# Kernel optimization log

Measured on AMD Instinct MI355X. Metric: run time of the kernel, lower is better.

## Reference

```python
import jax, jax.numpy as jnp
import numpy as np

B, N, D = 1024, 100000, 512


def setup_inputs() -> dict:
    key = jax.random.key(0)
    k1, k2, k3 = jax.random.split(key, 3)
    x_t = jax.random.normal(k1, (B, D), dtype=jnp.float32)
    # keep t away from 0/1 so b_t = 1 - t is well conditioned
    t = jax.random.uniform(k2, (B,), dtype=jnp.float32, minval=0.05, maxval=0.95)
    dataset = jax.random.normal(k3, (N, D), dtype=jnp.float32)
    return {"x_t": x_t, "t": t, "dataset": dataset}


def reference(x_t, t, dataset):
    # Straight-line AffineInterp: a_t = t, b_t = 1 - t, dot_a = 1, dot_b = -1.
    # Original detaches coeffs (detach=True).
    a_t = jax.lax.stop_gradient(t)
    b_t = jax.lax.stop_gradient(1.0 - t)
    dot_a_t = jnp.ones_like(a_t)
    dot_b_t = -jnp.ones_like(b_t)

    dataset_norm = jnp.sum(dataset * dataset, axis=1)          # (N,)
    term_1 = jnp.sum(x_t * x_t, axis=1)                        # (B,)
    term_2 = jnp.einsum('bd,nd->bn', x_t, dataset)             # (B, N)

    # ||x_t - a_t * x1||^2 expanded, scaled by -1/(2 b_t^2)
    logit = (term_1[:, None]
             - 2.0 * a_t[:, None] * term_2
             + (a_t * a_t)[:, None] * dataset_norm[None, :])
    logit = (-1.0 / (2.0 * b_t * b_t))[:, None] * logit        # (B, N)

    prob = jax.nn.softmax(logit, axis=1)                       # (B, N)
    data_coeff = dot_a_t - a_t * dot_b_t / b_t                 # (B,)
    prob = prob * data_coeff[:, None]

    weighted_dataset = jnp.einsum('bn,nd->bd', prob, dataset)  # (B, D)
    v = (dot_b_t / b_t)[:, None] * x_t + weighted_dataset
    return v
```

## Files before the change

### kernel.cpp

```cpp
#include <hip/hip_runtime.h>
#include <math.h>

#define B_SZ 1024
#define N_SZ 100000
#define D_SZ 512
#define NBLK 3125

typedef __attribute__((ext_vector_type(8))) short short8;
typedef __attribute__((ext_vector_type(16))) float float16;

__device__ __forceinline__ unsigned f2bf(float x) {
    unsigned u = __float_as_uint(x);
    u += 0x7FFFu + ((u >> 16) & 1u);
    return u >> 16;
}
__device__ __forceinline__ float bf2f(unsigned h) {
    return __uint_as_float(h << 16);
}

__global__ __launch_bounds__(256) void pre_kernel(
    const float* __restrict__ ds, const float* __restrict__ x_t,
    short* __restrict__ Yh, short* __restrict__ Yl, short* __restrict__ Yt,
    short* __restrict__ Xh, short* __restrict__ Xl, float* __restrict__ norms)
{
    __shared__ unsigned short YS[32 * 512];
    const int bx = blockIdx.x, tid = threadIdx.x;
    if (bx < NBLK) {
        const int row = tid >> 3, seg = tid & 7;
        const size_t g = (size_t)(bx * 32 + row) * 512 + seg * 64;
        const int ls = row * 512 + seg * 64;
        float nrm = 0.f;
        #pragma unroll
        for (int i = 0; i < 16; i++) {
            float4 v = *(const float4*)(ds + g + i * 4);
            nrm += v.x*v.x + v.y*v.y + v.z*v.z + v.w*v.w;
            unsigned h0 = f2bf(v.x), h1 = f2bf(v.y), h2 = f2bf(v.z), h3 = f2bf(v.w);
            unsigned l0 = f2bf(v.x - bf2f(h0)), l1 = f2bf(v.y - bf2f(h1));
            unsigned l2 = f2bf(v.z - bf2f(h2)), l3 = f2bf(v.w - bf2f(h3));
            uint2 hw = make_uint2(h0 | (h1 << 16), h2 | (h3 << 16));
            uint2 lw = make_uint2(l0 | (l1 << 16), l2 | (l3 << 16));
            *(uint2*)(Yh + g + i * 4) = hw;
            *(uint2*)(Yl + g + i * 4) = lw;
            *(uint2*)(YS + ls + i * 4) = hw;
        }
        nrm += __shfl_xor(nrm, 1, 64);
        nrm += __shfl_xor(nrm, 2, 64);
        nrm += __shfl_xor(nrm, 4, 64);
        if ((tid & 7) == 0) norms[bx * 32 + row] = nrm;
        __syncthreads();
        #pragma unroll
        for (int r = 0; r < 2; r++) {
            const int d = tid + r * 256;
            unsigned w[16];
            #pragma unroll
            for (int j = 0; j < 16; j++) {
                unsigned lo = YS[(2 * j) * 512 + d];
                unsigned hi = YS[(2 * j + 1) * 512 + d];
                w[j] = lo | (hi << 16);
            }
            uint4* dst = (uint4*)(Yt + (size_t)bx * 16384 + d * 32);
            dst[0] = make_uint4(w[0], w[1], w[2], w[3]);
            dst[1] = make_uint4(w[4], w[5], w[6], w[7]);
            dst[2] = make_uint4(w[8], w[9], w[10], w[11]);
            dst[3] = make_uint4(w[12], w[13], w[14], w[15]);
        }
    } else {
        const int xb = bx - NBLK;
        #pragma unroll
        for (int k = 0; k < 16; k++) {
            const size_t i4 = (size_t)xb * 4096 + k * 256 + tid;
            float4 v = *(const float4*)(x_t + i4 * 4);
            unsigned h0 = f2bf(v.x), h1 = f2bf(v.y), h2 = f2bf(v.z), h3 = f2bf(v.w);
            unsigned l0 = f2bf(v.x - bf2f(h0)), l1 = f2bf(v.y - bf2f(h1));
            unsigned l2 = f2bf(v.z - bf2f(h2)), l3 = f2bf(v.w - bf2f(h3));
            *(uint2*)(Xh + i4 * 4) = make_uint2(h0 | (h1 << 16), h2 | (h3 << 16));
            *(uint2*)(Xl + i4 * 4) = make_uint2(l0 | (l1 << 16), l2 | (l3 << 16));
        }
    }
}

__global__ __launch_bounds__(512, 2) void attn_kernel(
    const float* __restrict__ t,
    const short* __restrict__ Xh, const short* __restrict__ Xl,
    const short* __restrict__ Yh, const short* __restrict__ Yl,
    const short* __restrict__ Yt, const float* __restrict__ norms,
    float* __restrict__ m_part, float* __restrict__ l_part,
    float* __restrict__ acc_part, int chunk)
{
    __shared__ short YhL[32 * 512];
    __shared__ short YlL[32 * 512];
    __shared__ float slots[4 * 64 * 33];
    __shared__ float Pbuf[64 * 36];
    __shared__ float c1A[64], c2A[64], mAs[64], lAs[64], alA[64];
    __shared__ float nrmL[32];

    const int tid = threadIdx.x;
    const int wave = tid >> 6, lane = tid & 63;
    const int half = lane >> 5, l31 = lane & 31;

    int qbi = blockIdx.x, si = blockIdx.y;
    if (gridDim.x == 16 && gridDim.y == 16) {
        int fid = blockIdx.x + (blockIdx.y << 4);
        int xcd = fid & 7, slot = fid >> 3;
        si = xcd + ((slot & 1) << 3);
        qbi = slot >> 1;
    }
    const int qb = qbi * 64;
    const int s = si;
    const int n0s = s * chunk;
    const int n1 = min(N_SZ, n0s + chunk);
    const int numTiles = (n1 - n0s + 31) >> 5;

    if (tid < 64) {
        float tv = t[qb + tid];
        float bt = 1.0f - tv;
        float i2 = 1.0f / (2.0f * bt * bt);
        c1A[tid] = 2.0f * tv * i2;
        c2A[tid] = tv * tv * i2;
        mAs[tid] = -1e30f;
        lAs[tid] = 0.0f;
        alA[tid] = 0.0f;
    }
    __syncthreads();

    if (wave < 4) {
        short8 XF[2][8][2];
        #pragma unroll
        for (int qt = 0; qt < 2; qt++)
            #pragma unroll
            for (int kc = 0; kc < 8; kc++) {
                size_t off = (size_t)(qb + qt * 32 + l31) * 512 + wave * 128 + kc * 16 + half * 8;
                XF[qt][kc][0] = *(const short8*)(Xh + off);
                XF[qt][kc][1] = *(const short8*)(Xl + off);
            }

        for (int it = 0; it <= numTiles; ++it) {
            if (it < numTiles) {
                int n0 = n0s + it * 32;
                #pragma unroll
                for (int j = 0; j < 8; j++) {
                    int r = wave * 8 + j;
                    int gr = n0 + r;
                    if (gr < n1) {
                        const int gsw = (lane * 8) ^ ((r & 7) << 3);
                        const short* gh = Yh + (size_t)gr * 512 + gsw;
                        const short* gl = Yl + (size_t)gr * 512 + gsw;
                        __builtin_amdgcn_global_load_lds(
                            (const __attribute__((address_space(1))) unsigned int*)gh,
                            (__attribute__((address_space(3))) unsigned int*)&YhL[r * 512], 16, 0, 0);
                        __builtin_amdgcn_global_load_lds(
                            (const __attribute__((address_space(1))) unsigned int*)gl,
                            (__attribute__((address_space(3))) unsigned int*)&YlL[r * 512], 16, 0, 0);
                    } else {
                        short8 z;
                        #pragma unroll
                        for (int e = 0; e < 8; e++) z[e] = 0;
                        *(short8*)(&YhL[r * 512 + lane * 8]) = z;
                        *(short8*)(&YlL[r * 512 + lane * 8]) = z;
                    }
                }
                if (wave == 0 && lane < 32)
                    nrmL[lane] = (n0 + lane < n1) ? norms[n0 + lane] : 1e30f;
            }
            __syncthreads();

            if (it < numTiles) {
                float16 S0, S1;
                #pragma unroll
                for (int e = 0; e < 16; e++) { S0[e] = 0.f; S1[e] = 0.f; }
                #pragma unroll
                for (int kc = 0; kc < 8; kc++) {
                    const int koff = wave * 128 + kc * 16 + half * 8;
                    const int ksw = koff ^ ((l31 & 7) << 3);
                    short8 Ah = *(const short8*)(YhL + l31 * 512 + ksw);
                    short8 Al = *(const short8*)(YlL + l31 * 512 + ksw);
                    S0 = __builtin_amdgcn_mfma_f32_32x32x16_bf16(Ah, XF[0][kc][0], S0, 0, 0, 0);
                    S0 = __builtin_amdgcn_mfma_f32_32x32x16_bf16(Ah, XF[0][kc][1], S0, 0, 0, 0);
                    S0 = __builtin_amdgcn_mfma_f32_32x32x16_bf16(Al, XF[0][kc][0], S0, 0, 0, 0);
                    S1 = __builtin_amdgcn_mfma_f32_32x32x16_bf16(Ah, XF[1][kc][0], S1, 0, 0, 0);
                    S1 = __builtin_amdgcn_mfma_f32_32x32x16_bf16(Ah, XF[1][kc][1], S1, 0, 0, 0);
                    S1 = __builtin_amdgcn_mfma_f32_32x32x16_bf16(Al, XF[1][kc][0], S1, 0, 0, 0);
                }
                float* sb = &slots[wave * 2112];
                #pragma unroll
                for (int qt = 0; qt < 2; qt++) {
                    float* rowp = sb + (qt * 32 + l31) * 33;
                    #pragma unroll
                    for (int r = 0; r < 16; r++) {
                        int n = (r & 3) + 8 * (r >> 2) + 4 * half;
                        rowp[n] = qt ? S1[r] : S0[r];
                    }
                }
            }
            __syncthreads();

            if (it < numTiles) {
                int ql = lane >> 2, nq = lane & 3;
                int q = wave * 16 + ql;
                float c1q = c1A[q], c2q = c2A[q];
                float lg[8];
                float mt = -1e30f;
                #pragma unroll
                for (int j = 0; j < 8; j++) {
                    int n = nq * 8 + j;
                    float dd = slots[q * 33 + n] + slots[2112 + q * 33 + n]
                             + slots[4224 + q * 33 + n] + slots[6336 + q * 33 + n];
                    lg[j] = c1q * dd - c2q * nrmL[n];
                    mt = fmaxf(mt, lg[j]);
                }
                mt = fmaxf(mt, __shfl_xor(mt, 1, 64));
                mt = fmaxf(mt, __shfl_xor(mt, 2, 64));
                float mo = mAs[q];
                float mn = fmaxf(mo, mt);
                float al = __expf(mo - mn);
                float ls = 0.f;
                #pragma unroll
                for (int j = 0; j < 8; j++) {
                    float p = __expf(lg[j] - mn);
                    Pbuf[q * 36 + nq * 8 + j] = p;
                    ls += p;
                }
                ls += __shfl_xor(ls, 1, 64);
                ls += __shfl_xor(ls, 2, 64);
                if (nq == 0) {
                    mAs[q] = mn;
                    lAs[q] = lAs[q] * al + ls;
                    alA[q] = al;
                }
            }
            __syncthreads();
        }
        if (tid < 64) {
            m_part[(size_t)s * B_SZ + qb + tid] = mAs[tid];
            l_part[(size_t)s * B_SZ + qb + tid] = lAs[tid];
        }
    } else {
        const int dbase = (wave - 4) * 128;
        float16 O[4][2];
        #pragma unroll
        for (int dt = 0; dt < 4; dt++)
            #pragma unroll
            for (int qt = 0; qt < 2; qt++)
                #pragma unroll
                for (int e = 0; e < 16; e++) O[dt][qt][e] = 0.f;

        for (int it = 0; it <= numTiles; ++it) {
            __syncthreads();
            if (it > 0) {
                int blk = (n0s + (it - 1) * 32) >> 5;
                const short* yb = Yt + (size_t)blk * 16384;
                float al0 = alA[l31], al1 = alA[32 + l31];
                #pragma unroll
                for (int dt = 0; dt < 4; dt++) {
                    O[dt][0] *= al0;
                    O[dt][1] *= al1;
                }
                short8 AF[4][2];
                #pragma unroll
                for (int dt = 0; dt < 4; dt++)
                    #pragma unroll
                    for (int kc = 0; kc < 2; kc++)
                        AF[dt][kc] = *(const short8*)(yb + (dbase + dt * 32 + l31) * 32 + kc * 16 + half * 8);
                short8 BF[2][2];
                #pragma unroll
                for (int qt = 0; qt < 2; qt++)
                    #pragma unroll
                    for (int kc = 0; kc < 2; kc++) {
                        const float* pr = &Pbuf[(qt * 32 + l31) * 36 + kc * 16 + half * 8];
                        float4 pa = *(const float4*)pr;
                        float4 pb = *(const float4*)(pr + 4);
                        short8 b;
                        b[0] = (short)f2bf(pa.x); b[1] = (short)f2bf(pa.y);
                        b[2] = (short)f2bf(pa.z); b[3] = (short)f2bf(pa.w);
                        b[4] = (short)f2bf(pb.x); b[5] = (short)f2bf(pb.y);
                        b[6] = (short)f2bf(pb.z); b[7] = (short)f2bf(pb.w);
                        BF[qt][kc] = b;
                    }
                #pragma unroll
                for (int dt = 0; dt < 4; dt++)
                    #pragma unroll
                    for (int qt = 0; qt < 2; qt++)
                        #pragma unroll
                        for (int kc = 0; kc < 2; kc++)
                            O[dt][qt] = __builtin_amdgcn_mfma_f32_32x32x16_bf16(
                                AF[dt][kc], BF[qt][kc], O[dt][qt], 0, 0, 0);
            }
            __syncthreads();
            __syncthreads();
        }
        #pragma unroll
        for (int dt = 0; dt < 4; dt++)
            #pragma unroll
            for (int qt = 0; qt < 2; qt++) {
                int q = qb + qt * 32 + l31;
                float* op = acc_part + ((size_t)s * B_SZ + q) * D_SZ + dbase + dt * 32 + 4 * half;
                #pragma unroll
                for (int rg = 0; rg < 4; rg++) {
                    float4 v = make_float4(O[dt][qt][4 * rg], O[dt][qt][4 * rg + 1],
                                           O[dt][qt][4 * rg + 2], O[dt][qt][4 * rg + 3]);
                    *(float4*)(op + 8 * rg) = v;
                }
            }
    }
}

__global__ __launch_bounds__(256) void combine_kernel(
    const float* __restrict__ x_t, const float* __restrict__ t,
    const float* __restrict__ m_part, const float* __restrict__ l_part,
    const float* __restrict__ acc_part, float* __restrict__ out, int nsplit)
{
    int q = blockIdx.x;
    int tid = threadIdx.x;
    float M = -1e30f;
    for (int s = 0; s < nsplit; s++) M = fmaxf(M, m_part[(size_t)s * B_SZ + q]);
    float L = 0.f;
    for (int s = 0; s < nsplit; s++)
        L += l_part[(size_t)s * B_SZ + q] * __expf(m_part[(size_t)s * B_SZ + q] - M);

    float tv = t[q];
    float bt = 1.0f - tv;
    float coeff = 1.0f + tv / bt;
    float invb = 1.0f / bt;
    float invL = 1.0f / L;

    int d = tid * 2;
    float2 w = make_float2(0.f, 0.f);
    for (int s = 0; s < nsplit; s++) {
        float sc = __expf(m_part[(size_t)s * B_SZ + q] - M);
        float2 av = *(const float2*)(acc_part + ((size_t)s * B_SZ + q) * D_SZ + d);
        w.x += sc * av.x; w.y += sc * av.y;
    }
    float2 xv = *(const float2*)(x_t + (size_t)q * D_SZ + d);
    float2 o;
    o.x = -invb * xv.x + coeff * w.x * invL;
    o.y = -invb * xv.y + coeff * w.y * invL;
    *(float2*)(out + (size_t)q * D_SZ + d) = o;
}

extern "C" void kernel_launch(void* const* d_in, const int* in_sizes, int n_in,
                              void* d_out, int out_size, void* d_ws, size_t ws_size,
                              hipStream_t stream) {
    const float* x_t = (const float*)d_in[0];
    const float* t   = (const float*)d_in[1];
    const float* ds  = (const float*)d_in[2];
    float* out = (float*)d_out;

    short* wsS = (short*)d_ws;
    short* Yh = wsS;
    short* Yl = wsS + 51200000;
    short* Yt = wsS + 102400000;
    short* Xh = wsS + 153600000;
    short* Xl = wsS + 154124288;
    float* fbase = (float*)((char*)d_ws + 309297152);
    float* norms = fbase;
    int nsplit = 16;
    while (nsplit > 1 &&
           309697152ULL + (size_t)nsplit * 1024 * 4 * (2 + 512) > ws_size)
        nsplit >>= 1;
    float* m_part = fbase + 100000;
    float* l_part = m_part + (size_t)nsplit * B_SZ;
    float* acc    = l_part + (size_t)nsplit * B_SZ;
    int chunk = 32 * ((N_SZ + 32 * nsplit - 1) / (32 * nsplit));

    pre_kernel<<<dim3(NBLK + 32), dim3(256), 0, stream>>>(ds, x_t, Yh, Yl, Yt, Xh, Xl, norms);
    attn_kernel<<<dim3(16, nsplit), dim3(512), 0, stream>>>(
        t, Xh, Xl, Yh, Yl, Yt, norms, m_part, l_part, acc, chunk);
    combine_kernel<<<dim3(B_SZ), dim3(256), 0, stream>>>(
        x_t, t, m_part, l_part, acc, out, nsplit);
}
```

Baseline: 1.117 ms.

## Double-buffer Yh tiles in LDS and stream Yl fragments into registers

```diff
diff --git a/kernel.cpp b/kernel.cpp
--- a/kernel.cpp
+++ b/kernel.cpp
@@ -87,8 +87,7 @@
     float* __restrict__ m_part, float* __restrict__ l_part,
     float* __restrict__ acc_part, int chunk)
 {
-    __shared__ short YhL[32 * 512];
-    __shared__ short YlL[32 * 512];
+    __shared__ short YhL[2 * 32 * 512];
     __shared__ float slots[4 * 64 * 33];
     __shared__ float Pbuf[64 * 36];
     __shared__ float c1A[64], c2A[64], mAs[64], lAs[64], alA[64];
@@ -99,11 +98,12 @@
     const int half = lane >> 5, l31 = lane & 31;
 
     int qbi = blockIdx.x, si = blockIdx.y;
-    if (gridDim.x == 16 && gridDim.y == 16) {
-        int fid = blockIdx.x + (blockIdx.y << 4);
-        int xcd = fid & 7, slot = fid >> 3;
-        si = xcd + ((slot & 1) << 3);
-        qbi = slot >> 1;
+    if (gridDim.x == 16 && (gridDim.y & 7) == 0) {
+        int g = gridDim.y >> 3;
+        int fid = blockIdx.x + blockIdx.y * 16;
+        int xcd = fid & 7, j = fid >> 3;
+        si = xcd + 8 * (j % g);
+        qbi = j / g;
     }
     const int qb = qbi * 64;
     const int s = si;
@@ -121,7 +121,6 @@
         lAs[tid] = 0.0f;
         alA[tid] = 0.0f;
     }
-    __syncthreads();
 
     if (wave < 4) {
         short8 XF[2][8][2];
@@ -133,38 +132,44 @@
                 XF[qt][kc][0] = *(const short8*)(Xh + off);
                 XF[qt][kc][1] = *(const short8*)(Xl + off);
             }
+        {
+            #pragma unroll
+            for (int j = 0; j < 8; j++) {
+                int r = wave * 8 + j;
+                const int gsw = (lane * 8) ^ ((r & 7) << 3);
+                const short* gh = Yh + (size_t)(n0s + r) * 512 + gsw;
+                __builtin_amdgcn_global_load_lds(
+                    (const __attribute__((address_space(1))) unsigned int*)gh,
+                    (__attribute__((address_space(3))) unsigned int*)&YhL[r * 512], 16, 0, 0);
+            }
+        }
+        __syncthreads();
 
         for (int it = 0; it <= numTiles; ++it) {
+            short8 ALf[8];
             if (it < numTiles) {
-                int n0 = n0s + it * 32;
+                const int n0 = n0s + it * 32;
+                const short* ylrow = Yl + (size_t)(n0 + l31) * 512 + wave * 128 + half * 8;
+                #pragma unroll
+                for (int kc = 0; kc < 8; kc++)
+                    ALf[kc] = *(const short8*)(ylrow + kc * 16);
+                if (wave == 0 && lane < 32) nrmL[lane] = norms[n0 + lane];
+            }
+            if (it + 1 < numTiles) {
+                const int n0n = n0s + (it + 1) * 32;
+                short* dstb = YhL + ((it + 1) & 1) * (32 * 512);
                 #pragma unroll
                 for (int j = 0; j < 8; j++) {
                     int r = wave * 8 + j;
-                    int gr = n0 + r;
-                    if (gr < n1) {
-                        const int gsw = (lane * 8) ^ ((r & 7) << 3);
-                        const short* gh = Yh + (size_t)gr * 512 + gsw;
-                        const short* gl = Yl + (size_t)gr * 512 + gsw;
-                        __builtin_amdgcn_global_load_lds(
-                            (const __attribute__((address_space(1))) unsigned int*)gh,
-                            (__attribute__((address_space(3))) unsigned int*)&YhL[r * 512], 16, 0, 0);
-                        __builtin_amdgcn_global_load_lds(
-                            (const __attribute__((address_space(1))) unsigned int*)gl,
-                            (__attribute__((address_space(3))) unsigned int*)&YlL[r * 512], 16, 0, 0);
-                    } else {
-                        short8 z;
-                        #pragma unroll
-                        for (int e = 0; e < 8; e++) z[e] = 0;
-                        *(short8*)(&YhL[r * 512 + lane * 8]) = z;
-                        *(short8*)(&YlL[r * 512 + lane * 8]) = z;
-                    }
-                }
-                if (wave == 0 && lane < 32)
-                    nrmL[lane] = (n0 + lane < n1) ? norms[n0 + lane] : 1e30f;
-            }
-            __syncthreads();
-
+                    const int gsw = (lane * 8) ^ ((r & 7) << 3);
+                    const short* gh = Yh + (size_t)(n0n + r) * 512 + gsw;
+                    __builtin_amdgcn_global_load_lds(
+                        (const __attribute__((address_space(1))) unsigned int*)gh,
+                        (__attribute__((address_space(3))) unsigned int*)&dstb[r * 512], 16, 0, 0);
+                }
+            }
             if (it < numTiles) {
+                const short* Yb = YhL + (it & 1) * (32 * 512);
                 float16 S0, S1;
                 #pragma unroll
                 for (int e = 0; e < 16; e++) { S0[e] = 0.f; S1[e] = 0.f; }
@@ -172,14 +177,13 @@
                 for (int kc = 0; kc < 8; kc++) {
                     const int koff = wave * 128 + kc * 16 + half * 8;
                     const int ksw = koff ^ ((l31 & 7) << 3);
-                    short8 Ah = *(const short8*)(YhL + l31 * 512 + ksw);
-                    short8 Al = *(const short8*)(YlL + l31 * 512 + ksw);
+                    short8 Ah = *(const short8*)(Yb + l31 * 512 + ksw);
                     S0 = __builtin_amdgcn_mfma_f32_32x32x16_bf16(Ah, XF[0][kc][0], S0, 0, 0, 0);
                     S0 = __builtin_amdgcn_mfma_f32_32x32x16_bf16(Ah, XF[0][kc][1], S0, 0, 0, 0);
-                    S0 = __builtin_amdgcn_mfma_f32_32x32x16_bf16(Al, XF[0][kc][0], S0, 0, 0, 0);
+                    S0 = __builtin_amdgcn_mfma_f32_32x32x16_bf16(ALf[kc], XF[0][kc][0], S0, 0, 0, 0);
                     S1 = __builtin_amdgcn_mfma_f32_32x32x16_bf16(Ah, XF[1][kc][0], S1, 0, 0, 0);
                     S1 = __builtin_amdgcn_mfma_f32_32x32x16_bf16(Ah, XF[1][kc][1], S1, 0, 0, 0);
-                    S1 = __builtin_amdgcn_mfma_f32_32x32x16_bf16(Al, XF[1][kc][0], S1, 0, 0, 0);
+                    S1 = __builtin_amdgcn_mfma_f32_32x32x16_bf16(ALf[kc], XF[1][kc][0], S1, 0, 0, 0);
                 }
                 float* sb = &slots[wave * 2112];
                 #pragma unroll
@@ -244,23 +248,24 @@
                 #pragma unroll
                 for (int e = 0; e < 16; e++) O[dt][qt][e] = 0.f;
 
+        __syncthreads();
+
         for (int it = 0; it <= numTiles; ++it) {
-            __syncthreads();
             if (it > 0) {
                 int blk = (n0s + (it - 1) * 32) >> 5;
                 const short* yb = Yt + (size_t)blk * 16384;
-                float al0 = alA[l31], al1 = alA[32 + l31];
-                #pragma unroll
-                for (int dt = 0; dt < 4; dt++) {
-                    O[dt][0] *= al0;
-                    O[dt][1] *= al1;
-                }
                 short8 AF[4][2];
                 #pragma unroll
                 for (int dt = 0; dt < 4; dt++)
                     #pragma unroll
                     for (int kc = 0; kc < 2; kc++)
                         AF[dt][kc] = *(const short8*)(yb + (dbase + dt * 32 + l31) * 32 + kc * 16 + half * 8);
+                float al0 = alA[l31], al1 = alA[32 + l31];
+                #pragma unroll
+                for (int dt = 0; dt < 4; dt++) {
+                    O[dt][0] *= al0;
+                    O[dt][1] *= al1;
+                }
                 short8 BF[2][2];
                 #pragma unroll
                 for (int qt = 0; qt < 2; qt++)
```

Result: slower. 1.218 ms (+9.1%).
